# Kernel tuning notes

Measured on AMD Instinct MI355X. Metric: run time of the kernel, lower is better.

## Reference

```python
import jax, jax.numpy as jnp
import numpy as np

L = 32768      # sequence length
D_MODEL = 256  # input/output feature dim
D_HIDDEN = 256 # diagonal recurrent state dim
R_MIN, R_MAX, MAX_PHASE = 0.0, 1.0, 6.28


def setup_inputs() -> dict:
    key = jax.random.key(0)
    ks = jax.random.split(key, 8)
    inputs = jax.random.normal(ks[0], (L, D_MODEL), dtype=jnp.float32)
    # nu_init: log(-0.5*log(u*(r_max^2-r_min^2)+r_min^2))
    u1 = jax.random.uniform(ks[1], (D_HIDDEN,), dtype=jnp.float32)
    nu_log = jnp.log(-0.5 * jnp.log(u1 * (R_MAX**2 - R_MIN**2) + R_MIN**2))
    # theta_init: log(max_phase*u)
    u2 = jax.random.uniform(ks[2], (D_HIDDEN,), dtype=jnp.float32)
    theta_log = jnp.log(MAX_PHASE * u2)
    # gamma_log_init from (nu_log, theta_log)
    diag_lambda = jnp.exp(-jnp.exp(nu_log) + 1j * jnp.exp(theta_log))
    gamma_log = jnp.log(jnp.sqrt(1.0 - jnp.abs(diag_lambda) ** 2))
    bnorm = np.sqrt(2 * D_MODEL).astype(np.float32) if False else jnp.sqrt(2.0 * D_MODEL)
    cnorm = jnp.sqrt(2.0 * D_HIDDEN)
    B_re = jax.random.normal(ks[3], (D_HIDDEN, D_MODEL), dtype=jnp.float32) / bnorm
    B_im = jax.random.normal(ks[4], (D_HIDDEN, D_MODEL), dtype=jnp.float32) / bnorm
    C_re = jax.random.normal(ks[5], (D_MODEL, D_HIDDEN), dtype=jnp.float32) / cnorm
    C_im = jax.random.normal(ks[6], (D_MODEL, D_HIDDEN), dtype=jnp.float32) / cnorm
    D = jax.random.normal(ks[7], (D_MODEL,), dtype=jnp.float32)
    return {"inputs": inputs, "nu_log": nu_log, "theta_log": theta_log,
            "gamma_log": gamma_log, "B_re": B_re, "B_im": B_im,
            "C_re": C_re, "C_im": C_im, "D": D}


def _binop(q_i, q_j):
    # elementwise diagonal linear-recurrence combine
    A_i, b_i = q_i
    A_j, b_j = q_j
    return (A_j * A_i, A_j * b_i + b_j)


def reference(inputs, nu_log, theta_log, gamma_log, B_re, B_im, C_re, C_im, D):
    # h_{t+1} = lambda * h_t + B_norm x_{t+1};  y_t = Re[C h_t] + D * x_t
    diag_lambda = jnp.exp(-jnp.exp(nu_log) + 1j * jnp.exp(theta_log))  # (H,)
    B_norm = (B_re + 1j * B_im) * jnp.exp(gamma_log)[:, None]          # (H, M)
    C = C_re + 1j * C_im                                               # (M, H)
    Bu = inputs.astype(B_norm.dtype) @ B_norm.T                        # (L, H) complex
    Lam = jnp.broadcast_to(diag_lambda, (inputs.shape[0], diag_lambda.shape[0]))
    _, h = jax.lax.associative_scan(_binop, (Lam, Bu))                 # (L, H)
    return jnp.real(h @ C.T) + inputs * D                              # (L, M)
```

## Files before the change

### kernel.cpp

```cpp
#include <hip/hip_runtime.h>
#include <hip/hip_bf16.h>
#include <math.h>

#define LSEQ 32768
#define DMODEL 256
#define DHID 256
#define NCH 512
#define CHUNK 128
#define NCHUNKS (LSEQ / CHUNK)

typedef __bf16 bf16_t;
typedef _Float16 f16_t;
typedef __bf16 bf16x8 __attribute__((ext_vector_type(8)));
typedef __bf16 bf16x4 __attribute__((ext_vector_type(4)));
typedef float f32x4 __attribute__((ext_vector_type(4)));

__device__ __forceinline__ void async_load16(const void* g, void* l) {
  __builtin_amdgcn_global_load_lds((__attribute__((address_space(1))) void*)g,
                                   (__attribute__((address_space(3))) void*)l,
                                   16, 0, 0);
}

__device__ __forceinline__ float f16tof(unsigned int u) {
  return (float)__builtin_bit_cast(_Float16, (unsigned short)(u & 0xffffu));
}
__device__ __forceinline__ unsigned int fTobf(float f) {
  return (unsigned int)__builtin_bit_cast(unsigned short, (bf16_t)f);
}

__global__ void prep_all(const float* __restrict__ nu_log,
                         const float* __restrict__ theta_log,
                         const float* __restrict__ gamma_log,
                         const float* __restrict__ B_re, const float* __restrict__ B_im,
                         const float* __restrict__ C_re, const float* __restrict__ C_im,
                         const float* __restrict__ x,
                         float* __restrict__ lam, bf16_t* __restrict__ W1,
                         bf16_t* __restrict__ W2, bf16_t* __restrict__ xb) {
  const int bid = blockIdx.x, tid = threadIdx.x;
  if (bid == 0) {
    int h = tid;
    if (h < DHID) {
      double nu = exp((double)nu_log[h]);
      double th = exp((double)theta_log[h]);
#define PUT(row, n) { \
      double mag = exp(-(double)(n) * nu); \
      double ph  = fmod((double)(n) * th, 6.283185307179586); \
      lam[(row) * DHID + h]     = (float)(mag * cos(ph)); \
      lam[((row)+1) * DHID + h] = (float)(mag * sin(ph)); }
      PUT(0, 1.0)
      PUT(2, 32.0)
      for (int j = 0; j < 8; ++j) PUT(4 + 2 * j, 128.0 * (double)(1 << j))
#undef PUT
    }
  } else if (bid < 513) {
    int n = bid - 1, k = tid, h = n >> 1;
    float g = expf(gamma_log[h]);
    float v = (((n & 1) == 0) ? B_re[h * DMODEL + k] : B_im[h * DMODEL + k]) * g;
    W1[n * DMODEL + k] = (bf16_t)v;
  } else if (bid < 1025) {
    int idx = bid - 513;
    int m = idx >> 1, k = (idx & 1) * 256 + tid, h = k >> 1;
    float v = ((k & 1) == 0) ? C_re[m * DHID + h] : -C_im[m * DHID + h];
    W2[m * NCH + k] = (bf16_t)v;
  } else {
    int i = (bid - 1025) * 256 + tid;
    float4 v = ((const float4*)x)[i];
    bf16x4 o = {(bf16_t)v.x, (bf16_t)v.y, (bf16_t)v.z, (bf16_t)v.w};
    ((bf16x4*)xb)[i] = o;
  }
}

__global__ __launch_bounds__(512) void gemm1_scan(
    const bf16_t* __restrict__ A, const bf16_t* __restrict__ Bw,
    f16_t* __restrict__ Bu, const float* __restrict__ lam,
    float* __restrict__ E) {
  __shared__ __align__(16) char smem[69632];
  bf16_t* As = (bf16_t*)smem;
  bf16_t* Bs = (bf16_t*)(smem + 8192);
  char*   Bt = smem;
  float*  Ep = (float*)(smem + 65536);

  const int tid = threadIdx.x;
  const int gx = blockIdx.x;
  const int c  = blockIdx.y;
  const int r0 = c * CHUNK;
  const int c0 = gx * 256;
  const int wave = tid >> 6, lane = tid & 63;
  const int wm = wave & 1, wn = wave >> 1;
  const int lrow = lane & 15, lk = lane >> 4;
  const int ra = tid >> 2, ka = (tid & 3) * 8;

  f32x4 acc[4][4] = {};

  for (int k0 = 0; k0 < DMODEL; k0 += 32) {
    __syncthreads();
    async_load16(A + (size_t)(r0 + ra) * DMODEL + k0 + ka, (char*)As + tid * 16);
    async_load16(Bw + (size_t)(c0 + ra) * DMODEL + k0 + ka, (char*)Bs + tid * 16);
    async_load16(Bw + (size_t)(c0 + 128 + ra) * DMODEL + k0 + ka,
                 (char*)Bs + 8192 + tid * 16);
    __syncthreads();
    bf16x8 af[4], bfr[4];
#pragma unroll
    for (int i = 0; i < 4; ++i)
      af[i] = *(const bf16x8*)(As + (wm * 64 + i * 16 + lrow) * 32 + lk * 8);
#pragma unroll
    for (int j = 0; j < 4; ++j)
      bfr[j] = *(const bf16x8*)(Bs + (wn * 64 + j * 16 + lrow) * 32 + lk * 8);
#pragma unroll
    for (int i = 0; i < 4; ++i)
#pragma unroll
      for (int j = 0; j < 4; ++j)
        acc[i][j] = __builtin_amdgcn_mfma_f32_16x16x32_bf16(af[i], bfr[j], acc[i][j], 0, 0, 0);
  }
  __syncthreads();

#pragma unroll
  for (int i = 0; i < 4; ++i)
#pragma unroll
    for (int r = 0; r < 4; ++r) {
      int row = wm * 64 + i * 16 + lk * 4 + r;
      int key = (row & 7) << 4;
#pragma unroll
      for (int j = 0; j < 4; ++j) {
        int col = wn * 64 + j * 16 + lrow;
        *(f16_t*)(Bt + row * 512 + ((col * 2) ^ key)) = (f16_t)acc[i][j][r];
      }
    }
  __syncthreads();

  char* dst = (char*)Bu + (size_t)r0 * 1024 + gx * 512;
#pragma unroll
  for (int it = 0; it < 8; ++it) {
    int idx = it * 512 + tid;
    int row = idx >> 5, off = (idx & 31) * 16;
    *(f32x4*)(dst + (size_t)row * 1024 + off) = *(const f32x4*)(Bt + row * 512 + off);
  }

  {
    int p = tid & 127, seg = tid >> 7;
    int h = gx * 128 + p;
    float lre = lam[h], lim = lam[DHID + h];
    float sre = 0.f, sim = 0.f;
    int cb = 4 * p;
#pragma unroll 4
    for (int t = 0; t < 32; ++t) {
      int row = seg * 32 + t;
      unsigned int w = *(const unsigned int*)(Bt + row * 512 + (cb ^ ((row & 7) << 4)));
      float bre = f16tof(w), bim = f16tof(w >> 16);
      float nre = fmaf(lre, sre, fmaf(-lim, sim, bre));
      float nim = fmaf(lre, sim, fmaf(lim, sre, bim));
      sre = nre; sim = nim;
    }
    Ep[seg * 256 + 2 * p]     = sre;
    Ep[seg * 256 + 2 * p + 1] = sim;
  }
  __syncthreads();
  if (tid < 128) {
    int p = tid, h = gx * 128 + p;
    float ar = lam[2 * DHID + h], ai = lam[3 * DHID + h];
    float er = Ep[2 * p], ei = Ep[2 * p + 1];
#pragma unroll
    for (int s = 1; s < 4; ++s) {
      float tr = fmaf(ar, er, fmaf(-ai, ei, Ep[s * 256 + 2 * p]));
      float ti = fmaf(ar, ei, fmaf(ai, er, Ep[s * 256 + 2 * p + 1]));
      er = tr; ei = ti;
    }
    E[(size_t)c * NCH + 2 * h]     = er;
    E[(size_t)c * NCH + 2 * h + 1] = ei;
  }
}

__global__ __launch_bounds__(512) void scan_gemm2(
    const f16_t* __restrict__ Bu, const bf16_t* __restrict__ W2,
    const float* __restrict__ lam, const float* __restrict__ E,
    const float* __restrict__ X, const float* __restrict__ Dv,
    float* __restrict__ out) {
  __shared__ __align__(16) char smem[147456];
  char*   H  = smem;
  bf16_t* Bs = (bf16_t*)(smem + 131072);
  float*  Ep = (float*)(smem + 131072);

  const int tid = threadIdx.x;
  const int c = (int)gridDim.x - 1 - (int)blockIdx.x;
  const int r0 = c * CHUNK;

  const char* src = (const char*)Bu + (size_t)r0 * 1024;
#pragma unroll
  for (int it = 0; it < 16; ++it)
    async_load16(src + it * 8192 + tid * 16, H + it * 8192 + tid * 16);

  {
    int p = tid & 255, half = tid >> 8;
    int m = c >> 1;
    int lo = half ? m : 0, end = half ? c : m;
    float aR = lam[4 * DHID + p], aI = lam[5 * DHID + p];
    float sr = 0.f, si = 0.f;
#pragma unroll 4
    for (int k = lo; k < end; ++k) {
      float2 e = *(const float2*)(E + (size_t)k * NCH + 2 * p);
      float nr = fmaf(aR, sr, fmaf(-aI, si, e.x));
      float ni = fmaf(aR, si, fmaf(aI, sr, e.y));
      sr = nr; si = ni;
    }
    Ep[half * 512 + 2 * p]     = sr;
    Ep[half * 512 + 2 * p + 1] = si;
  }
  __syncthreads();

  if (tid < 256) {
    int p = tid;
    int lenb = c - (c >> 1);
    float pr = 1.f, pi = 0.f;
#pragma unroll
    for (int j = 0; j < 8; ++j)
      if (lenb & (1 << j)) {
        float br = lam[(4 + 2 * j) * DHID + p], bi = lam[(5 + 2 * j) * DHID + p];
        float nr = pr * br - pi * bi, ni = pr * bi + pi * br;
        pr = nr; pi = ni;
      }
    float sar = Ep[2 * p], sai = Ep[2 * p + 1];
    float sbr = Ep[512 + 2 * p], sbi = Ep[512 + 2 * p + 1];
    float carR = fmaf(pr, sar, fmaf(-pi, sai, sbr));
    float carI = fmaf(pr, sai, fmaf(pi, sar, sbi));

    float lre = lam[p], lim = lam[DHID + p];
    float sre = carR, sim = carI;
    int cb = 4 * p;
#pragma unroll 4
    for (int t = 0; t < CHUNK; ++t) {
      unsigned int* ptr = (unsigned int*)(H + t * 1024 + (cb ^ ((t & 7) << 4)));
      unsigned int w = *ptr;
      float bre = f16tof(w), bim = f16tof(w >> 16);
      float nre = fmaf(lre, sre, fmaf(-lim, sim, bre));
      float nim = fmaf(lre, sim, fmaf(lim, sre, bim));
      sre = nre; sim = nim;
      *ptr = (fTobf(sim) << 16) | fTobf(sre);
    }
  }

  const int wave = tid >> 6, lane = tid & 63;
  const int wm = wave & 1, wn = wave >> 1;
  const int lrow = lane & 15, lk = lane >> 4;
  const int ra = tid >> 2, ka = (tid & 3) * 8;
  f32x4 acc[4][4] = {};
  for (int k0 = 0; k0 < NCH; k0 += 32) {
    __syncthreads();
#pragma unroll
    for (int it = 0; it < 2; ++it) {
      int idx = it * 512 + tid;
      async_load16(W2 + (size_t)(idx >> 2) * NCH + k0 + (idx & 3) * 8,
                   (char*)Bs + idx * 16);
    }
    __syncthreads();
    bf16x8 af[4], bfr[4];
#pragma unroll
    for (int i = 0; i < 4; ++i) {
      int m = wm * 64 + i * 16 + lrow;
      af[i] = *(const bf16x8*)(H + m * 1024 + ((2 * k0 + lk * 16) ^ ((m & 7) << 4)));
    }
#pragma unroll
    for (int j = 0; j < 4; ++j)
      bfr[j] = *(const bf16x8*)(Bs + (wn * 64 + j * 16 + lrow) * 32 + lk * 8);
#pragma unroll
    for (int i = 0; i < 4; ++i)
#pragma unroll
      for (int j = 0; j < 4; ++j)
        acc[i][j] = __builtin_amdgcn_mfma_f32_16x16x32_bf16(af[i], bfr[j], acc[i][j], 0, 0, 0);
  }

#pragma unroll
  for (int i = 0; i < 4; ++i)
#pragma unroll
    for (int r = 0; r < 4; ++r) {
      int row = r0 + wm * 64 + i * 16 + lk * 4 + r;
#pragma unroll
      for (int j = 0; j < 4; ++j) {
        int col = wn * 64 + j * 16 + lrow;
        float v = acc[i][j][r] + X[(size_t)row * DMODEL + col] * Dv[col];
        out[(size_t)row * DMODEL + col] = v;
      }
    }
}

extern "C" void kernel_launch(void* const* d_in, const int* in_sizes, int n_in,
                              void* d_out, int out_size, void* d_ws, size_t ws_size,
                              hipStream_t stream) {
  const float* inputs    = (const float*)d_in[0];
  const float* nu_log    = (const float*)d_in[1];
  const float* theta_log = (const float*)d_in[2];
  const float* gamma_log = (const float*)d_in[3];
  const float* B_re      = (const float*)d_in[4];
  const float* B_im      = (const float*)d_in[5];
  const float* C_re      = (const float*)d_in[6];
  const float* C_im      = (const float*)d_in[7];
  const float* Dvec      = (const float*)d_in[8];
  float* out = (float*)d_out;

  char* w = (char*)d_ws;
  bf16_t* W1 = (bf16_t*)w; w += (size_t)NCH * DMODEL * 2;
  bf16_t* W2 = (bf16_t*)w; w += (size_t)DMODEL * NCH * 2;
  float* lam = (float*)w;  w += 24576;
  bf16_t* xb = (bf16_t*)w; w += (size_t)LSEQ * DMODEL * 2;
  f16_t* Bu  = (f16_t*)w;  w += (size_t)LSEQ * NCH * 2;
  float* E   = (float*)w;  w += (size_t)NCHUNKS * NCH * 4;

  prep_all<<<9217, 256, 0, stream>>>(nu_log, theta_log, gamma_log,
                                     B_re, B_im, C_re, C_im, inputs,
                                     lam, W1, W2, xb);
  gemm1_scan<<<dim3(2, NCHUNKS), 512, 0, stream>>>(xb, W1, Bu, lam, E);
  scan_gemm2<<<NCHUNKS, 512, 0, stream>>>(Bu, W2, lam, E, inputs, Dvec, out);
}
```

Before: 157.1 us.

## Fuse input bf16 conversion into GEMM1 and parallelize intra-chunk scan across 1024 threads

Removes the separate x-to-bf16 pass in the prep kernel. GEMM1 now loads fp32 inputs directly, converts them in registers and stores them to LDS, which saves a full round trip of a bf16 copy through global memory. In scan_gemm2 the block grows to 1024 threads and the 128-step sequential scan per state is split into four 32-step segments: local partial sums, a carry combine using lambda^32, then a rescan. The GEMM2 tiling is adjusted to 16 waves. The trade-off is extra scan work, more syncs and more LDS, and GEMM1's A loads are no longer asynchronous.

```diff
diff --git a/kernel.cpp b/kernel.cpp
--- a/kernel.cpp
+++ b/kernel.cpp
@@ -12,7 +12,6 @@
 typedef __bf16 bf16_t;
 typedef _Float16 f16_t;
 typedef __bf16 bf16x8 __attribute__((ext_vector_type(8)));
-typedef __bf16 bf16x4 __attribute__((ext_vector_type(4)));
 typedef float f32x4 __attribute__((ext_vector_type(4)));
 
 __device__ __forceinline__ void async_load16(const void* g, void* l) {
@@ -33,9 +32,8 @@
                          const float* __restrict__ gamma_log,
                          const float* __restrict__ B_re, const float* __restrict__ B_im,
                          const float* __restrict__ C_re, const float* __restrict__ C_im,
-                         const float* __restrict__ x,
                          float* __restrict__ lam, bf16_t* __restrict__ W1,
-                         bf16_t* __restrict__ W2, bf16_t* __restrict__ xb) {
+                         bf16_t* __restrict__ W2) {
   const int bid = blockIdx.x, tid = threadIdx.x;
   if (bid == 0) {
     int h = tid;
@@ -57,21 +55,16 @@
     float g = expf(gamma_log[h]);
     float v = (((n & 1) == 0) ? B_re[h * DMODEL + k] : B_im[h * DMODEL + k]) * g;
     W1[n * DMODEL + k] = (bf16_t)v;
-  } else if (bid < 1025) {
+  } else {
     int idx = bid - 513;
     int m = idx >> 1, k = (idx & 1) * 256 + tid, h = k >> 1;
     float v = ((k & 1) == 0) ? C_re[m * DHID + h] : -C_im[m * DHID + h];
     W2[m * NCH + k] = (bf16_t)v;
-  } else {
-    int i = (bid - 1025) * 256 + tid;
-    float4 v = ((const float4*)x)[i];
-    bf16x4 o = {(bf16_t)v.x, (bf16_t)v.y, (bf16_t)v.z, (bf16_t)v.w};
-    ((bf16x4*)xb)[i] = o;
   }
 }
 
 __global__ __launch_bounds__(512) void gemm1_scan(
-    const bf16_t* __restrict__ A, const bf16_t* __restrict__ Bw,
+    const float* __restrict__ X, const bf16_t* __restrict__ Bw,
     f16_t* __restrict__ Bu, const float* __restrict__ lam,
     float* __restrict__ E) {
   __shared__ __align__(16) char smem[69632];
@@ -93,11 +86,16 @@
   f32x4 acc[4][4] = {};
 
   for (int k0 = 0; k0 < DMODEL; k0 += 32) {
+    const float* xrow = X + (size_t)(r0 + ra) * DMODEL + k0 + ka;
+    float4 a0 = ((const float4*)xrow)[0];
+    float4 a1 = ((const float4*)xrow)[1];
     __syncthreads();
-    async_load16(A + (size_t)(r0 + ra) * DMODEL + k0 + ka, (char*)As + tid * 16);
     async_load16(Bw + (size_t)(c0 + ra) * DMODEL + k0 + ka, (char*)Bs + tid * 16);
     async_load16(Bw + (size_t)(c0 + 128 + ra) * DMODEL + k0 + ka,
                  (char*)Bs + 8192 + tid * 16);
+    bf16x8 av = {(bf16_t)a0.x, (bf16_t)a0.y, (bf16_t)a0.z, (bf16_t)a0.w,
+                 (bf16_t)a1.x, (bf16_t)a1.y, (bf16_t)a1.z, (bf16_t)a1.w};
+    *(bf16x8*)(As + ra * 32 + ka) = av;
     __syncthreads();
     bf16x8 af[4], bfr[4];
 #pragma unroll
@@ -170,15 +168,17 @@
   }
 }
 
-__global__ __launch_bounds__(512) void scan_gemm2(
+__global__ __launch_bounds__(1024) void scan_gemm2(
     const f16_t* __restrict__ Bu, const bf16_t* __restrict__ W2,
     const float* __restrict__ lam, const float* __restrict__ E,
     const float* __restrict__ X, const float* __restrict__ Dv,
     float* __restrict__ out) {
-  __shared__ __align__(16) char smem[147456];
+  __shared__ __align__(16) char smem[155648];
   char*   H  = smem;
   bf16_t* Bs = (bf16_t*)(smem + 131072);
-  float*  Ep = (float*)(smem + 131072);
+  float*  LB = (float*)(smem + 131072);
+  float*  Pp = (float*)(smem + 135168);
+  float*  Tt = (float*)(smem + 147456);
 
   const int tid = threadIdx.x;
   const int c = (int)gridDim.x - 1 - (int)blockIdx.x;
@@ -186,10 +186,10 @@
 
   const char* src = (const char*)Bu + (size_t)r0 * 1024;
 #pragma unroll
-  for (int it = 0; it < 16; ++it)
-    async_load16(src + it * 8192 + tid * 16, H + it * 8192 + tid * 16);
-
-  {
+  for (int it = 0; it < 8; ++it)
+    async_load16(src + it * 16384 + tid * 16, H + it * 16384 + tid * 16);
+
+  if (tid < 512) {
     int p = tid & 255, half = tid >> 8;
     int m = c >> 1;
     int lo = half ? m : 0, end = half ? c : m;
@@ -202,8 +202,27 @@
       float ni = fmaf(aR, si, fmaf(aI, sr, e.y));
       sr = nr; si = ni;
     }
-    Ep[half * 512 + 2 * p]     = sr;
-    Ep[half * 512 + 2 * p + 1] = si;
+    LB[half * 512 + 2 * p]     = sr;
+    LB[half * 512 + 2 * p + 1] = si;
+  }
+  __syncthreads();
+
+  {
+    int p = tid & 255, seg = tid >> 8;
+    float lre = lam[p], lim = lam[DHID + p];
+    float sre = 0.f, sim = 0.f;
+    int cb = 4 * p;
+#pragma unroll 4
+    for (int t = 0; t < 32; ++t) {
+      int row = seg * 32 + t;
+      unsigned int w = *(const unsigned int*)(H + row * 1024 + (cb ^ ((row & 7) << 4)));
+      float bre = f16tof(w), bim = f16tof(w >> 16);
+      float nre = fmaf(lre, sre, fmaf(-lim, sim, bre));
+      float nim = fmaf(lre, sim, fmaf(lim, sre, bim));
+      sre = nre; sim = nim;
+    }
+    Pp[seg * 512 + 2 * p]     = sre;
+    Pp[seg * 512 + 2 * p + 1] = sim;
   }
   __syncthreads();
 
@@ -218,17 +237,32 @@
         float nr = pr * br - pi * bi, ni = pr * bi + pi * br;
         pr = nr; pi = ni;
       }
-    float sar = Ep[2 * p], sai = Ep[2 * p + 1];
-    float sbr = Ep[512 + 2 * p], sbi = Ep[512 + 2 * p + 1];
-    float carR = fmaf(pr, sar, fmaf(-pi, sai, sbr));
-    float carI = fmaf(pr, sai, fmaf(pi, sar, sbi));
-
+    float sar = LB[2 * p], sai = LB[2 * p + 1];
+    float sbr = LB[512 + 2 * p], sbi = LB[512 + 2 * p + 1];
+    float tr = fmaf(pr, sar, fmaf(-pi, sai, sbr));
+    float ti = fmaf(pr, sai, fmaf(pi, sar, sbi));
+    float l32r = lam[2 * DHID + p], l32i = lam[3 * DHID + p];
+    Tt[2 * p] = tr; Tt[2 * p + 1] = ti;
+#pragma unroll
+    for (int s = 1; s < 4; ++s) {
+      float pR = Pp[(s - 1) * 512 + 2 * p], pI = Pp[(s - 1) * 512 + 2 * p + 1];
+      float nr = fmaf(l32r, tr, fmaf(-l32i, ti, pR));
+      float ni = fmaf(l32r, ti, fmaf(l32i, tr, pI));
+      tr = nr; ti = ni;
+      Tt[s * 512 + 2 * p] = tr; Tt[s * 512 + 2 * p + 1] = ti;
+    }
+  }
+  __syncthreads();
+
+  {
+    int p = tid & 255, seg = tid >> 8;
     float lre = lam[p], lim = lam[DHID + p];
-    float sre = carR, sim = carI;
+    float sre = Tt[seg * 512 + 2 * p], sim = Tt[seg * 512 + 2 * p + 1];
     int cb = 4 * p;
 #pragma unroll 4
-    for (int t = 0; t < CHUNK; ++t) {
-      unsigned int* ptr = (unsigned int*)(H + t * 1024 + (cb ^ ((t & 7) << 4)));
+    for (int t = 0; t < 32; ++t) {
+      int row = seg * 32 + t;
+      unsigned int* ptr = (unsigned int*)(H + row * 1024 + (cb ^ ((row & 7) << 4)));
       unsigned int w = *ptr;
       float bre = f16tof(w), bim = f16tof(w >> 16);
       float nre = fmaf(lre, sre, fmaf(-lim, sim, bre));
@@ -239,40 +273,35 @@
   }
 
   const int wave = tid >> 6, lane = tid & 63;
-  const int wm = wave & 1, wn = wave >> 1;
+  const int wm = wave & 3, wn = wave >> 2;
   const int lrow = lane & 15, lk = lane >> 4;
-  const int ra = tid >> 2, ka = (tid & 3) * 8;
-  f32x4 acc[4][4] = {};
+  f32x4 acc[2][4] = {};
   for (int k0 = 0; k0 < NCH; k0 += 32) {
     __syncthreads();
-#pragma unroll
-    for (int it = 0; it < 2; ++it) {
-      int idx = it * 512 + tid;
-      async_load16(W2 + (size_t)(idx >> 2) * NCH + k0 + (idx & 3) * 8,
-                   (char*)Bs + idx * 16);
-    }
+    async_load16(W2 + (size_t)(tid >> 2) * NCH + k0 + (tid & 3) * 8,
+                 (char*)Bs + tid * 16);
     __syncthreads();
-    bf16x8 af[4], bfr[4];
-#pragma unroll
-    for (int i = 0; i < 4; ++i) {
-      int m = wm * 64 + i * 16 + lrow;
+    bf16x8 af[2], bfr[4];
+#pragma unroll
+    for (int i = 0; i < 2; ++i) {
+      int m = wm * 32 + i * 16 + lrow;
       af[i] = *(const bf16x8*)(H + m * 1024 + ((2 * k0 + lk * 16) ^ ((m & 7) << 4)));
     }
 #pragma unroll
     for (int j = 0; j < 4; ++j)
       bfr[j] = *(const bf16x8*)(Bs + (wn * 64 + j * 16 + lrow) * 32 + lk * 8);
 #pragma unroll
-    for (int i = 0; i < 4; ++i)
+    for (int i = 0; i < 2; ++i)
 #pragma unroll
       for (int j = 0; j < 4; ++j)
         acc[i][j] = __builtin_amdgcn_mfma_f32_16x16x32_bf16(af[i], bfr[j], acc[i][j], 0, 0, 0);
   }
 
 #pragma unroll
-  for (int i = 0; i < 4; ++i)
+  for (int i = 0; i < 2; ++i)
 #pragma unroll
     for (int r = 0; r < 4; ++r) {
-      int row = r0 + wm * 64 + i * 16 + lk * 4 + r;
+      int row = r0 + wm * 32 + i * 16 + lk * 4 + r;
 #pragma unroll
       for (int j = 0; j < 4; ++j) {
         int col = wn * 64 + j * 16 + lrow;
@@ -300,13 +329,12 @@
   bf16_t* W1 = (bf16_t*)w; w += (size_t)NCH * DMODEL * 2;
   bf16_t* W2 = (bf16_t*)w; w += (size_t)DMODEL * NCH * 2;
   float* lam = (float*)w;  w += 24576;
-  bf16_t* xb = (bf16_t*)w; w += (size_t)LSEQ * DMODEL * 2;
   f16_t* Bu  = (f16_t*)w;  w += (size_t)LSEQ * NCH * 2;
   float* E   = (float*)w;  w += (size_t)NCHUNKS * NCH * 4;
 
-  prep_all<<<9217, 256, 0, stream>>>(nu_log, theta_log, gamma_log,
-                                     B_re, B_im, C_re, C_im, inputs,
-                                     lam, W1, W2, xb);
-  gemm1_scan<<<dim3(2, NCHUNKS), 512, 0, stream>>>(xb, W1, Bu, lam, E);
-  scan_gemm2<<<NCHUNKS, 512, 0, stream>>>(Bu, W2, lam, E, inputs, Dvec, out);
-}
+  prep_all<<<1025, 256, 0, stream>>>(nu_log, theta_log, gamma_log,
+                                     B_re, B_im, C_re, C_im,
+                                     lam, W1, W2);
+  gemm1_scan<<<dim3(2, NCHUNKS), 512, 0, stream>>>(inputs, W1, Bu, lam, E);
+  scan_gemm2<<<NCHUNKS, 1024, 0, stream>>>(Bu, W2, lam, E, inputs, Dvec, out);
+}
```

Result: no change. 155.3 us (-1.1%).
